# Kernel optimization log

Hardware: AMD Instinct MI355X
Metric: run time of the kernel (lower is better)

Reference implementation:

```python
import jax, jax.numpy as jnp
import numpy as np

V, H, B, S, T = 512, 1024, 128, 256, 128


def setup_inputs() -> dict:
    key = jax.random.key(0)
    ks = jax.random.split(key, 16)
    s = 1.0 / np.sqrt(H)
    f32 = jnp.float32
    return {
        "encoder_outputs": jax.random.normal(ks[0], (B, S, H), f32),
        "encoder_hidden": jax.random.normal(ks[1], (1, B, H), f32),
        "encoder_cell": jax.random.normal(ks[2], (1, B, H), f32),
        "target_tensor": jax.random.randint(ks[3], (B, T), 0, V),
        "max_length": T,
        "emb": (jax.random.normal(ks[4], (V, H), f32) * s),
        "Wa_w": jax.random.normal(ks[5], (H, H), f32) * s,
        "Wa_b": jnp.zeros((H,), f32),
        "Ua_w": jax.random.normal(ks[6], (H, H), f32) * s,
        "Ua_b": jnp.zeros((H,), f32),
        "Va_w": jax.random.normal(ks[7], (1, H), f32) * s,
        "Va_b": jnp.zeros((1,), f32),
        "W_ih": jax.random.normal(ks[8], (4 * H, 2 * H), f32) * s,
        "W_hh": jax.random.normal(ks[9], (4 * H, H), f32) * s,
        "b_ih": jnp.zeros((4 * H,), f32),
        "b_hh": jnp.zeros((4 * H,), f32),
        "out_w": jax.random.normal(ks[10], (V, H), f32) * s,
        "out_b": jnp.zeros((V,), f32),
    }


def reference(encoder_outputs, encoder_hidden, encoder_cell, target_tensor, max_length,
              emb, Wa_w, Wa_b, Ua_w, Ua_b, Va_w, Va_b,
              W_ih, W_hh, b_ih, b_hh, out_w, out_b):
    # Teacher forcing: decoder input at step i is SOS (=0) then target[:, i-1].
    bsz = encoder_outputs.shape[0]
    sos = jnp.zeros((bsz, 1), dtype=target_tensor.dtype)
    tokens = jnp.concatenate([sos, target_tensor[:, : max_length - 1]], axis=1)  # [B, T]
    xs = emb[tokens].transpose(1, 0, 2)  # [T, B, H] (dropout = identity, eval mode)

    # Ua(keys) is loop-invariant (original recomputes it each step; same math).
    keys_proj = jnp.einsum('bsh,kh->bsk', encoder_outputs, Ua_w) + Ua_b  # [B, S, H]

    def step(carry, emb_t):
        h, c = carry  # [B, H] each
        q = h @ Wa_w.T + Wa_b  # Bahdanau query projection [B, H]
        e = jnp.tanh(q[:, None, :] + keys_proj) @ Va_w[0] + Va_b[0]  # [B, S]
        w = jax.nn.softmax(e, axis=-1)
        ctx = jnp.einsum('bs,bsh->bh', w, encoder_outputs)
        x = jnp.concatenate([emb_t, ctx], axis=-1)  # [B, 2H]
        gates = x @ W_ih.T + b_ih + h @ W_hh.T + b_hh  # [B, 4H], torch order i,f,g,o
        i, f, g, o = jnp.split(gates, 4, axis=-1)
        c_new = jax.nn.sigmoid(f) * c + jax.nn.sigmoid(i) * jnp.tanh(g)
        h_new = jax.nn.sigmoid(o) * jnp.tanh(c_new)
        logits = h_new @ out_w.T + out_b  # [B, V]
        return (h_new, c_new), (logits, w)

    init = (encoder_hidden[0], encoder_cell[0])
    (h_fin, c_fin), (logits, attn) = jax.lax.scan(step, init, xs)
    log_probs = jax.nn.log_softmax(logits.transpose(1, 0, 2), axis=-1)  # [B, T, V]
    return log_probs, h_fin[None], attn.transpose(1, 0, 2)  # hidden [1,B,H], attn [B,T,S]
```

## Files before the change

kernel.cpp:

```cpp
#include <hip/hip_runtime.h>

#define B_ 128
#define S_ 256
#define H_ 1024
#define V_ 512
#define T_ 128
#define G4 4096

typedef __attribute__((ext_vector_type(8))) short bf16x8;
typedef __attribute__((ext_vector_type(4))) float f32x4;
typedef __attribute__((ext_vector_type(2))) float f32x2;

__device__ __forceinline__ float bf2f(unsigned short x) {
    unsigned int u = ((unsigned int)x) << 16;
    return __builtin_bit_cast(float, u);
}
__device__ __forceinline__ unsigned short f2b(float f) {
    unsigned int u = __builtin_bit_cast(unsigned int, f);
    u = u + 0x7fffu + ((u >> 16) & 1u);
    return (unsigned short)(u >> 16);
}
__device__ __forceinline__ float ftanh(float x) {
    float e = __expf(2.f * x);
    return 1.f - 2.f * __builtin_amdgcn_rcpf(e + 1.f);
}
__device__ __forceinline__ float fsigm(float x) {
    return __builtin_amdgcn_rcpf(1.f + __expf(-x));
}
__device__ __forceinline__ void gll16(const void* g, void* l) {
    __builtin_amdgcn_global_load_lds(
        (const __attribute__((address_space(1))) unsigned int*)g,
        (__attribute__((address_space(3))) unsigned int*)l, 16, 0, 0);
}

__device__ __forceinline__ unsigned char sw_e4m3(float f) {
    unsigned int ub = __builtin_bit_cast(unsigned int, f);
    unsigned char s = (unsigned char)((ub >> 24) & 0x80);
    float a = fabsf(f);
    if (!(a < 464.f)) return (unsigned char)(s | 0x7E);
    if (a < 0.0009765625f) return s;
    if (a < 0.015625f) {
        int m = (int)(a * 512.f + 0.5f);
        if (m >= 8) return (unsigned char)(s | 0x08);
        return (unsigned char)(s | m);
    }
    unsigned int u = __builtin_bit_cast(unsigned int, a);
    u += 0x7FFFF + ((u >> 20) & 1);
    int e = (int)(u >> 23) - 127;
    if (e > 8) return (unsigned char)(s | 0x7E);
    unsigned int man = (u >> 20) & 7;
    return (unsigned char)(s | ((unsigned int)(e + 7) << 3) | man);
}
__device__ __forceinline__ float sw_f_e4m3(unsigned int byte) {
    unsigned int s = (byte & 0x80u) << 24;
    unsigned int em = byte & 0x7Fu;
    float v;
    if (em >= 8u) v = __builtin_bit_cast(float, (em + 960u) << 20);
    else v = (float)em * 0.001953125f;
    return __builtin_bit_cast(float, __builtin_bit_cast(unsigned int, v) | s);
}
__device__ __forceinline__ unsigned char enc1(float a) {
#if __has_builtin(__builtin_amdgcn_cvt_pk_fp8_f32)
    unsigned int w = __builtin_amdgcn_cvt_pk_fp8_f32(a, a, 0u, false);
    return (unsigned char)(w & 0xff);
#else
    return sw_e4m3(a);
#endif
}
__device__ __forceinline__ unsigned int enc4(float a, float b, float c, float d) {
#if __has_builtin(__builtin_amdgcn_cvt_pk_fp8_f32)
    unsigned int w = 0;
    w = __builtin_amdgcn_cvt_pk_fp8_f32(a, b, w, false);
    w = __builtin_amdgcn_cvt_pk_fp8_f32(c, d, w, true);
    return w;
#else
    return (unsigned int)sw_e4m3(a) | ((unsigned int)sw_e4m3(b) << 8) |
           ((unsigned int)sw_e4m3(c) << 16) | ((unsigned int)sw_e4m3(d) << 24);
#endif
}
__device__ __forceinline__ void dec4(unsigned int w, float* o) {
#if __has_builtin(__builtin_amdgcn_cvt_pk_f32_fp8)
    f32x2 lo = __builtin_amdgcn_cvt_pk_f32_fp8(w, false);
    f32x2 hi = __builtin_amdgcn_cvt_pk_f32_fp8(w, true);
    o[0] = lo.x; o[1] = lo.y; o[2] = hi.x; o[3] = hi.y;
#else
    o[0] = sw_f_e4m3(w & 0xff); o[1] = sw_f_e4m3((w >> 8) & 0xff);
    o[2] = sw_f_e4m3((w >> 16) & 0xff); o[3] = sw_f_e4m3(w >> 24);
#endif
}

__global__ void f32_to_bf16_x4(const float4* __restrict__ in, ushort4* __restrict__ out, int n4) {
    int i = blockIdx.x * 256 + threadIdx.x;
    if (i < n4) {
        float4 v = in[i];
        ushort4 o;
        o.x = f2b(v.x); o.y = f2b(v.y); o.z = f2b(v.z); o.w = f2b(v.w);
        out[i] = o;
    }
}

__global__ void f32_to_fp8_x4(const float4* __restrict__ in, unsigned int* __restrict__ out, int n4) {
    int i = blockIdx.x * 256 + threadIdx.x;
    if (i < n4) {
        float4 v = in[i];
        out[i] = enc4(v.x, v.y, v.z, v.w);
    }
}

__global__ void cvt_gather(const float* __restrict__ src, int src_ld, int coff,
                           unsigned short* __restrict__ dst, int perm) {
    int i = blockIdx.x * 256 + threadIdx.x;
    int r = i >> 8;
    int c = (i & 255) * 4;
    int sr = perm ? (((r & 3) << 10) + (r >> 2)) : r;
    float4 v = *reinterpret_cast<const float4*>(src + (size_t)sr * src_ld + coff + c);
    ushort4 o;
    o.x = f2b(v.x); o.y = f2b(v.y); o.z = f2b(v.z); o.w = f2b(v.w);
    *reinterpret_cast<ushort4*>(dst + (size_t)r * 1024 + c) = o;
}

__global__ void build_toks(const int* __restrict__ target, int* __restrict__ toks) {
    int idx = blockIdx.x * 256 + threadIdx.x;
    if (idx < T_ * B_) {
        int t = idx / B_, b = idx % B_;
        toks[idx] = (t == 0) ? 0 : target[b * T_ + t - 1];
    }
}

__global__ void build_bsum(const float* __restrict__ b_ih, const float* __restrict__ b_hh,
                           float* __restrict__ bsum) {
    int j = blockIdx.x * 256 + threadIdx.x;
    if (j < G4) {
        int pj = ((j & 3) << 10) + (j >> 2);
        bsum[j] = b_ih[pj] + b_hh[pj];
    }
}

template<int MODE>
__global__ __launch_bounds__(256) void gemm_mf(
    const unsigned short* __restrict__ A,
    const unsigned short* __restrict__ Bw,
    int K, int ldb, int ldc,
    float* __restrict__ C, unsigned char* __restrict__ C8,
    const float* __restrict__ bias)
{
    __shared__ unsigned short As[2 * 8192];
    __shared__ unsigned short Bs[2 * 8192];
    const int tid = threadIdx.x;
    const int lane = tid & 63;
    const int wv = tid >> 6;
    const int m0 = blockIdx.x * 64;
    const int n0 = blockIdx.y * 64;

    const unsigned short* ga[4];
    const unsigned short* gb[4];
    #pragma unroll
    for (int j = 0; j < 4; ++j) {
        int ci = tid + 256 * j;
        int row = ci >> 4;
        int src = (ci & 15) ^ (row & 7);
        ga[j] = A + (size_t)(m0 + row) * K + src * 8;
        gb[j] = Bw + (size_t)(n0 + row) * ldb + src * 8;
    }

    f32x4 acc[2][2] = {};
    const int r0 = (wv >> 1) * 32;
    const int cq0 = (wv & 1) * 32;
    const int fr = lane & 15;
    const int kg = lane >> 4;

    auto stage = [&](int k0, int p) {
        #pragma unroll
        for (int j = 0; j < 4; ++j) {
            gll16(ga[j] + k0, As + p * 8192 + j * 2048 + wv * 512);
            gll16(gb[j] + k0, Bs + p * 8192 + j * 2048 + wv * 512);
        }
    };

    stage(0, 0);
    stage(128, 1);
    int p = 0;
    for (int k0 = 0; k0 < K; k0 += 128) {
        if (k0 + 128 < K) {
            asm volatile("s_waitcnt vmcnt(8)" ::: "memory");
        } else {
            asm volatile("s_waitcnt vmcnt(0)" ::: "memory");
        }
        __builtin_amdgcn_sched_barrier(0);
        __builtin_amdgcn_s_barrier();
        __builtin_amdgcn_sched_barrier(0);
        const unsigned short* Ab = As + p * 8192;
        const unsigned short* Bb = Bs + p * 8192;
        bf16x8 af[2][4], bfr[2][4];
        #pragma unroll
        for (int f = 0; f < 2; ++f)
            #pragma unroll
            for (int kh = 0; kh < 4; ++kh) {
                int ra = r0 + f * 16 + fr;
                af[f][kh] = *(const bf16x8*)&Ab[ra * 128 + (((kh * 4 + kg) ^ (ra & 7)) << 3)];
                int rb = cq0 + f * 16 + fr;
                bfr[f][kh] = *(const bf16x8*)&Bb[rb * 128 + (((kh * 4 + kg) ^ (rb & 7)) << 3)];
            }
        asm volatile("s_waitcnt lgkmcnt(0)" ::: "memory");
        __builtin_amdgcn_sched_barrier(0);
        __builtin_amdgcn_s_barrier();
        __builtin_amdgcn_sched_barrier(0);
        if (k0 + 256 < K) stage(k0 + 256, p);
        __builtin_amdgcn_s_setprio(1);
        #pragma unroll
        for (int f = 0; f < 2; ++f)
            #pragma unroll
            for (int g = 0; g < 2; ++g)
                #pragma unroll
                for (int kh = 0; kh < 4; ++kh)
                    acc[f][g] = __builtin_amdgcn_mfma_f32_16x16x32_bf16(
                        af[f][kh], bfr[g][kh], acc[f][g], 0, 0, 0);
        __builtin_amdgcn_s_setprio(0);
        p ^= 1;
    }

    const int erow = (lane >> 4) * 4;
    const int ecol = lane & 15;
    #pragma unroll
    for (int f = 0; f < 2; ++f) {
        #pragma unroll
        for (int g = 0; g < 2; ++g) {
            #pragma unroll
            for (int r = 0; r < 4; ++r) {
                int row = m0 + r0 + f * 16 + erow + r;
                int col = n0 + cq0 + g * 16 + ecol;
                float v = acc[f][g][r] + bias[col];
                if (MODE == 0) C[(size_t)row * ldc + col] = v;
                else C8[(size_t)row * ldc + col] = enc1(v);
            }
        }
    }
}

template<int MODE>
__global__ __launch_bounds__(256) void gemm_n32(
    const unsigned short* __restrict__ A,
    const unsigned short* __restrict__ Bw,
    int K, int ldb, int ldc,
    float* __restrict__ C, unsigned short* __restrict__ Cb,
    const float* __restrict__ bias,
    const float* __restrict__ Pemb,
    const int* __restrict__ toks,
    float* __restrict__ Cq,
    float* __restrict__ Lg,
    int flag)
{
    __shared__ unsigned short As[3 * 8192];
    __shared__ unsigned short Bs[3 * 4096];
    const int tid = threadIdx.x;
    const int lane = tid & 63;
    const int wv = tid >> 6;
    const int m0 = blockIdx.x * 64;
    const int n0 = blockIdx.y * 32;

    const unsigned short* ga[4];
    const unsigned short* gb[2];
    #pragma unroll
    for (int j = 0; j < 4; ++j) {
        int ci = tid + 256 * j;
        int row = ci >> 4;
        int src = (ci & 15) ^ (row & 7);
        ga[j] = A + (size_t)(m0 + row) * K + src * 8;
    }
    #pragma unroll
    for (int j = 0; j < 2; ++j) {
        int ci = tid + 256 * j;
        int row = ci >> 4;
        int src = (ci & 15) ^ (row & 7);
        gb[j] = Bw + (size_t)(n0 + row) * ldb + src * 8;
    }

    f32x4 acc[2] = {};
    const int r0 = (wv >> 1) * 32;
    const int c0 = (wv & 1) * 16;
    const int fr = lane & 15;
    const int kg = lane >> 4;

    auto stage = [&](int k0, int p) {
        #pragma unroll
        for (int j = 0; j < 4; ++j)
            gll16(ga[j] + k0, As + p * 8192 + j * 2048 + wv * 512);
        #pragma unroll
        for (int j = 0; j < 2; ++j)
            gll16(gb[j] + k0, Bs + p * 4096 + j * 2048 + wv * 512);
    };

    stage(0, 0);
    stage(128, 1);
    stage(256, 2);
    int p = 0;
    for (int k0 = 0; k0 < K; k0 += 128) {
        if (k0 + 256 < K) {
            asm volatile("s_waitcnt vmcnt(12)" ::: "memory");
        } else if (k0 + 128 < K) {
            asm volatile("s_waitcnt vmcnt(6)" ::: "memory");
        } else {
            asm volatile("s_waitcnt vmcnt(0)" ::: "memory");
        }
        __builtin_amdgcn_sched_barrier(0);
        __builtin_amdgcn_s_barrier();
        __builtin_amdgcn_sched_barrier(0);
        const unsigned short* Ab = As + p * 8192;
        const unsigned short* Bb = Bs + p * 4096;
        bf16x8 af[2][4], bfr[4];
        #pragma unroll
        for (int kh = 0; kh < 4; ++kh) {
            #pragma unroll
            for (int f = 0; f < 2; ++f) {
                int ra = r0 + f * 16 + fr;
                af[f][kh] = *(const bf16x8*)&Ab[ra * 128 + (((kh * 4 + kg) ^ (ra & 7)) << 3)];
            }
            int rb = c0 + fr;
            bfr[kh] = *(const bf16x8*)&Bb[rb * 128 + (((kh * 4 + kg) ^ (rb & 7)) << 3)];
        }
        asm volatile("s_waitcnt lgkmcnt(0)" ::: "memory");
        __builtin_amdgcn_sched_barrier(0);
        __builtin_amdgcn_s_barrier();
        __builtin_amdgcn_sched_barrier(0);
        if (k0 + 384 < K) stage(k0 + 384, p);
        __builtin_amdgcn_s_setprio(1);
        #pragma unroll
        for (int f = 0; f < 2; ++f)
            #pragma unroll
            for (int kh = 0; kh < 4; ++kh)
                acc[f] = __builtin_amdgcn_mfma_f32_16x16x32_bf16(
                    af[f][kh], bfr[kh], acc[f], 0, 0, 0);
        __builtin_amdgcn_s_setprio(0);
        p = (p == 2) ? 0 : p + 1;
    }

    const int erow = (lane >> 4) * 4;
    const int ecol = lane & 15;

    if constexpr (MODE == 4) {
        __shared__ float Lt[64 * 32];
        __syncthreads();
        #pragma unroll
        for (int f = 0; f < 2; ++f)
            #pragma unroll
            for (int r = 0; r < 4; ++r)
                Lt[(r0 + f * 16 + erow + r) * 32 + c0 + ecol] = acc[f][r];
        __syncthreads();
        #pragma unroll
        for (int i = 0; i < 2; ++i) {
            int pi = tid + 256 * i;
            int r = pi >> 3, u = pi & 7;
            int b = m0 + r;
            int hh = (n0 >> 2) + u;
            f32x4 gv = *reinterpret_cast<const f32x4*>(&Lt[r * 32 + u * 4]);
            const float* gp = C + (size_t)b * G4 + n0 + u * 4;
            float iv = gv[0] + gp[0];
            float fv = gv[1] + gp[1];
            float gg = gv[2] + gp[2];
            float ov = gv[3] + gp[3];
            int ci = b * H_ + hh;
            float cn = fsigm(fv) * Cq[ci] + fsigm(iv) * ftanh(gg);
            float hn = fsigm(ov) * ftanh(cn);
            Cq[ci] = cn;
            Cb[ci] = f2b(hn);
            if (flag) Lg[ci] = hn;
        }
    } else {
        #pragma unroll
        for (int f = 0; f < 2; ++f) {
            #pragma unroll
            for (int r = 0; r < 4; ++r) {
                int row = m0 + r0 + f * 16 + erow + r;
                int col = n0 + c0 + ecol;
                float v = acc[f][r];
                if (MODE == 0) {
                    C[(size_t)row * ldc + col] = v + bias[col];
                } else {
                    if (col < H_) {
                        Cq[(size_t)row * H_ + col] = v + bias[col];
                    } else {
                        int cg = col - H_;
                        C[(size_t)row * G4 + cg] = v + Pemb[(size_t)toks[row] * G4 + cg];
                    }
                }
            }
        }
    }
}

__global__ __launch_bounds__(256) void attn_e(
    const unsigned int* __restrict__ kp8,
    const float* __restrict__ q,
    const float* __restrict__ Va,
    const unsigned int* __restrict__ encb8,
    float* __restrict__ es_g,
    unsigned short* __restrict__ pctx)
{
    const int b = blockIdx.x;
    const int sh = blockIdx.y;
    const int tid = threadIdx.x;
    const int lane = tid & 63;
    const int wv = tid >> 6;
    __shared__ float qs[H_];
    __shared__ float vas[H_];
    __shared__ float pe[16];

    *reinterpret_cast<float4*>(&qs[tid * 4]) =
        *reinterpret_cast<const float4*>(&q[(size_t)b * H_ + tid * 4]);
    *reinterpret_cast<float4*>(&vas[tid * 4]) =
        *reinterpret_cast<const float4*>(&Va[tid * 4]);
    __syncthreads();

    #pragma unroll
    for (int si = 0; si < 4; ++si) {
        int s_loc = wv * 4 + si;
        const uint4* kr = reinterpret_cast<const uint4*>(
            kp8 + (size_t)(b * S_ + sh * 16 + s_loc) * 256);
        uint4 u = kr[lane];
        const int h0 = lane * 16;
        float d[4];
        float acc = 0.f;
        dec4(u.x, d);
        acc += vas[h0 + 0] * ftanh(qs[h0 + 0] + d[0]);
        acc += vas[h0 + 1] * ftanh(qs[h0 + 1] + d[1]);
        acc += vas[h0 + 2] * ftanh(qs[h0 + 2] + d[2]);
        acc += vas[h0 + 3] * ftanh(qs[h0 + 3] + d[3]);
        dec4(u.y, d);
        acc += vas[h0 + 4] * ftanh(qs[h0 + 4] + d[0]);
        acc += vas[h0 + 5] * ftanh(qs[h0 + 5] + d[1]);
        acc += vas[h0 + 6] * ftanh(qs[h0 + 6] + d[2]);
        acc += vas[h0 + 7] * ftanh(qs[h0 + 7] + d[3]);
        dec4(u.z, d);
        acc += vas[h0 + 8] * ftanh(qs[h0 + 8] + d[0]);
        acc += vas[h0 + 9] * ftanh(qs[h0 + 9] + d[1]);
        acc += vas[h0 + 10] * ftanh(qs[h0 + 10] + d[2]);
        acc += vas[h0 + 11] * ftanh(qs[h0 + 11] + d[3]);
        dec4(u.w, d);
        acc += vas[h0 + 12] * ftanh(qs[h0 + 12] + d[0]);
        acc += vas[h0 + 13] * ftanh(qs[h0 + 13] + d[1]);
        acc += vas[h0 + 14] * ftanh(qs[h0 + 14] + d[2]);
        acc += vas[h0 + 15] * ftanh(qs[h0 + 15] + d[3]);
        #pragma unroll
        for (int off = 32; off; off >>= 1) acc += __shfl_down(acc, off);
        if (lane == 0) {
            pe[s_loc] = __expf(acc);
            es_g[(size_t)b * S_ + sh * 16 + s_loc] = acc;
        }
    }
    __syncthreads();

    const int c0 = tid * 4;
    float ax = 0.f, ay = 0.f, az = 0.f, aw = 0.f;
    #pragma unroll
    for (int sl = 0; sl < 16; ++sl) {
        unsigned int u = encb8[(size_t)(b * S_ + sh * 16 + sl) * 256 + tid];
        float d[4];
        dec4(u, d);
        float w = pe[sl];
        ax += w * d[0];
        ay += w * d[1];
        az += w * d[2];
        aw += w * d[3];
    }
    ushort4 o4;
    o4.x = f2b(ax); o4.y = f2b(ay); o4.z = f2b(az); o4.w = f2b(aw);
    *reinterpret_cast<ushort4*>(&pctx[((size_t)b * 16 + sh) * H_ + c0]) = o4;
}

__global__ __launch_bounds__(256) void attn_comb(
    const float* __restrict__ es_g,
    const unsigned short* __restrict__ pctx,
    unsigned short* __restrict__ ctxb,
    float* __restrict__ attnOut,
    int t)
{
    const int b = blockIdx.x;
    const int hh = blockIdx.y;
    const int tid = threadIdx.x;
    const int lane = tid & 63;
    const int wv = tid >> 6;
    __shared__ float reds[4];

    float ex = __expf(es_g[(size_t)b * S_ + tid]);
    float sm = ex;
    #pragma unroll
    for (int off = 32; off; off >>= 1) sm += __shfl_xor(sm, off);
    if (lane == 0) reds[wv] = sm;
    __syncthreads();
    sm = reds[0] + reds[1] + reds[2] + reds[3];
    float rZ = __builtin_amdgcn_rcpf(sm);
    if (hh == 0) attnOut[((size_t)(b * T_ + t)) * S_ + tid] = ex * rZ;

    const int c0 = hh * 512 + tid * 2;
    float a0 = 0.f, a1 = 0.f;
    #pragma unroll
    for (int blk = 0; blk < 16; ++blk) {
        ushort2 pv = *reinterpret_cast<const ushort2*>(
            &pctx[((size_t)b * 16 + blk) * H_ + c0]);
        a0 += bf2f(pv.x); a1 += bf2f(pv.y);
    }
    ushort2 o; o.x = f2b(a0 * rZ); o.y = f2b(a1 * rZ);
    *reinterpret_cast<ushort2*>(&ctxb[(size_t)b * H_ + c0]) = o;
}

__global__ __launch_bounds__(256) void lsm_all(
    const float* __restrict__ lgall,
    float* __restrict__ lp)
{
    int r = blockIdx.x;
    int t = r >> 7, b = r & (B_ - 1);
    int tid = threadIdx.x;
    int lane = tid & 63, wv = tid >> 6;
    __shared__ float red[4];
    float a0 = lgall[(size_t)r * V_ + tid];
    float a1 = lgall[(size_t)r * V_ + 256 + tid];
    float mx = fmaxf(a0, a1);
    #pragma unroll
    for (int off = 32; off; off >>= 1) mx = fmaxf(mx, __shfl_xor(mx, off));
    if (lane == 0) red[wv] = mx;
    __syncthreads();
    mx = fmaxf(fmaxf(red[0], red[1]), fmaxf(red[2], red[3]));
    float sm = __expf(a0 - mx) + __expf(a1 - mx);
    #pragma unroll
    for (int off = 32; off; off >>= 1) sm += __shfl_xor(sm, off);
    __syncthreads();
    if (lane == 0) red[wv] = sm;
    __syncthreads();
    sm = red[0] + red[1] + red[2] + red[3];
    float lse = mx + __logf(sm);
    size_t off = ((size_t)b * T_ + t) * V_;
    lp[off + tid] = a0 - lse;
    lp[off + tid + 256] = a1 - lse;
}

extern "C" void kernel_launch(void* const* d_in, const int* in_sizes, int n_in,
                              void* d_out, int out_size, void* d_ws, size_t ws_size,
                              hipStream_t stream) {
    const float* enc   = (const float*)d_in[0];
    const float* h0    = (const float*)d_in[1];
    const float* c0    = (const float*)d_in[2];
    const int*   targ  = (const int*)d_in[3];
    const float* emb   = (const float*)d_in[5];
    const float* Wa_w  = (const float*)d_in[6];
    const float* Wa_b  = (const float*)d_in[7];
    const float* Ua_w  = (const float*)d_in[8];
    const float* Ua_b  = (const float*)d_in[9];
    const float* Va_w  = (const float*)d_in[10];
    const float* W_ih  = (const float*)d_in[12];
    const float* W_hh  = (const float*)d_in[13];
    const float* b_ih  = (const float*)d_in[14];
    const float* b_hh  = (const float*)d_in[15];
    const float* out_w = (const float*)d_in[16];
    const float* out_b = (const float*)d_in[17];

    float* out  = (float*)d_out;
    float* lp   = out;
    float* hid  = out + (size_t)B_ * T_ * V_;
    float* attn = hid + (size_t)B_ * H_;

    char* w = (char*)d_ws;
    auto alloc = [&](size_t bytes) {
        char* p = w;
        w += (bytes + 255) & ~(size_t)255;
        return p;
    };
    const size_t NKP = (size_t)B_ * S_ * H_;
    unsigned int* kp8      = (unsigned int*)alloc(NKP);
    unsigned int* encb8    = (unsigned int*)alloc(NKP);
    char* uni = alloc(NKP * 2);
    unsigned short* encb = (unsigned short*)uni;
    unsigned short* hall = (unsigned short*)uni;
    float* lgall = (float*)(uni + (size_t)T_ * B_ * H_ * 2);
    unsigned short* Wcat_b = (unsigned short*)alloc((size_t)5120 * H_ * 2);
    unsigned short* Wih1_b = (unsigned short*)alloc((size_t)G4 * H_ * 2);
    unsigned short* Wih2_b = (unsigned short*)alloc((size_t)G4 * H_ * 2);
    unsigned short* Uaw_b  = (unsigned short*)alloc((size_t)H_ * H_ * 2);
    unsigned short* emb_b  = (unsigned short*)alloc((size_t)V_ * H_ * 2);
    unsigned short* owb_b  = (unsigned short*)alloc((size_t)V_ * H_ * 2);
    unsigned short* hb0    = (unsigned short*)alloc((size_t)B_ * H_ * 2);
    unsigned short* ctxb   = (unsigned short*)alloc((size_t)B_ * H_ * 2);
    float* Pemb  = (float*)alloc((size_t)V_ * G4 * 4);
    float* bsumP = (float*)alloc((size_t)G4 * 4);
    int*   toks  = (int*)alloc((size_t)T_ * B_ * 4);
    float* cbuf  = (float*)alloc((size_t)B_ * H_ * 4);
    float* qbuf  = (float*)alloc((size_t)B_ * H_ * 4);
    float* gates = (float*)alloc((size_t)B_ * G4 * 4);
    float* es_g  = (float*)alloc((size_t)B_ * S_ * 4);
    unsigned short* pctx = (unsigned short*)alloc((size_t)B_ * 16 * H_ * 2);
    if ((size_t)(w - (char*)d_ws) > ws_size) return;

    auto cvt = [&](const float* src, unsigned short* dst, size_t n) {
        int n4 = (int)(n / 4);
        f32_to_bf16_x4<<<(n4 + 255) / 256, 256, 0, stream>>>((const float4*)src, (ushort4*)dst, n4);
    };

    cvt(enc, encb, NKP);
    f32_to_fp8_x4<<<(int)(NKP / 4 + 255) / 256, 256, 0, stream>>>(
        (const float4*)enc, encb8, (int)(NKP / 4));
    cvt(Ua_w, Uaw_b, (size_t)H_ * H_);
    cvt(emb, emb_b, (size_t)V_ * H_);
    cvt(h0, hb0, (size_t)B_ * H_);
    cvt_gather<<<1024, 256, 0, stream>>>(Wa_w, H_, 0, Wcat_b, 0);
    cvt_gather<<<4096, 256, 0, stream>>>(W_hh, H_, 0, Wcat_b + (size_t)1024 * H_, 1);
    cvt_gather<<<512, 256, 0, stream>>>(out_w, H_, 0, owb_b, 0);
    cvt_gather<<<4096, 256, 0, stream>>>(W_ih, 2 * H_, 0, Wih1_b, 1);
    cvt_gather<<<4096, 256, 0, stream>>>(W_ih, 2 * H_, H_, Wih2_b, 1);
    build_toks<<<(T_ * B_ + 255) / 256, 256, 0, stream>>>(targ, toks);
    build_bsum<<<(G4 + 255) / 256, 256, 0, stream>>>(b_ih, b_hh, bsumP);
    hipMemcpyAsync(cbuf, c0, (size_t)B_ * H_ * 4, hipMemcpyDeviceToDevice, stream);

    gemm_mf<1><<<dim3((B_ * S_) / 64, H_ / 64), 256, 0, stream>>>(
        encb, Uaw_b, H_, H_, H_, nullptr, (unsigned char*)kp8, Ua_b);
    gemm_mf<0><<<dim3(V_ / 64, G4 / 64), 256, 0, stream>>>(
        emb_b, Wih1_b, H_, H_, G4, Pemb, nullptr, bsumP);

    for (int t = 0; t < T_; ++t) {
        const unsigned short* hprev = (t == 0) ? hb0 : hall + (size_t)(t - 1) * B_ * H_;
        gemm_n32<2><<<dim3(2, 160), 256, 0, stream>>>(
            hprev, Wcat_b, H_, H_, 0, gates, nullptr, Wa_b,
            Pemb, toks + t * B_, qbuf, nullptr, 0);
        attn_e<<<dim3(B_, 16), 256, 0, stream>>>(kp8, qbuf, Va_w, encb8, es_g, pctx);
        attn_comb<<<dim3(B_, 2), 256, 0, stream>>>(es_g, pctx, ctxb, attn, t);
        gemm_n32<4><<<dim3(2, 128), 256, 0, stream>>>(
            ctxb, Wih2_b, H_, H_, 0, gates, hall + (size_t)t * B_ * H_, nullptr,
            nullptr, nullptr, cbuf, hid, t == T_ - 1);
    }

    gemm_n32<0><<<dim3((T_ * B_) / 64, V_ / 32), 256, 0, stream>>>(
        hall, owb_b, H_, H_, V_, lgall, nullptr, out_b,
        nullptr, nullptr, nullptr, nullptr, 0);
    lsm_all<<<T_ * B_, 256, 0, stream>>>(lgall, lp);
}
```

Before: 5.612 ms.

## Fuse attention score, softmax and context into one kernel per batch half

Replaces the two-kernel attention (partial scores/context per 16-position slice, then a combine kernel) with a single kernel where each block handles one batch row and half of the hidden dimension, computing all 256 scores, the softmax and the context in place. This removes one launch per decoder step and the global round trip through partial-context and score buffers. The score/tanh work is now duplicated across the two half-blocks per batch row, and the grid shrinks from 2048 to 256 blocks, reducing parallelism.

```diff
diff --git a/kernel.cpp b/kernel.cpp
--- a/kernel.cpp
+++ b/kernel.cpp
@@ -388,35 +388,36 @@
     }
 }
 
-__global__ __launch_bounds__(256) void attn_e(
+__global__ __launch_bounds__(512) void attn_fused(
     const unsigned int* __restrict__ kp8,
     const float* __restrict__ q,
     const float* __restrict__ Va,
     const unsigned int* __restrict__ encb8,
-    float* __restrict__ es_g,
-    unsigned short* __restrict__ pctx)
+    unsigned short* __restrict__ ctxb,
+    float* __restrict__ attnOut,
+    int t)
 {
-    const int b = blockIdx.x;
-    const int sh = blockIdx.y;
+    const int b = blockIdx.x >> 1;
+    const int hh = blockIdx.x & 1;
     const int tid = threadIdx.x;
     const int lane = tid & 63;
     const int wv = tid >> 6;
     __shared__ float qs[H_];
     __shared__ float vas[H_];
-    __shared__ float pe[16];
-
-    *reinterpret_cast<float4*>(&qs[tid * 4]) =
-        *reinterpret_cast<const float4*>(&q[(size_t)b * H_ + tid * 4]);
-    *reinterpret_cast<float4*>(&vas[tid * 4]) =
-        *reinterpret_cast<const float4*>(&Va[tid * 4]);
-    __syncthreads();
-
-    #pragma unroll
-    for (int si = 0; si < 4; ++si) {
-        int s_loc = wv * 4 + si;
-        const uint4* kr = reinterpret_cast<const uint4*>(
-            kp8 + (size_t)(b * S_ + sh * 16 + s_loc) * 256);
-        uint4 u = kr[lane];
+    __shared__ float es[S_];
+    __shared__ float red[8];
+    __shared__ float part[4][128][4];
+
+    *reinterpret_cast<float2*>(&qs[tid * 2]) =
+        *reinterpret_cast<const float2*>(&q[(size_t)b * H_ + tid * 2]);
+    *reinterpret_cast<float2*>(&vas[tid * 2]) =
+        *reinterpret_cast<const float2*>(&Va[tid * 2]);
+    __syncthreads();
+
+    for (int si = 0; si < 32; ++si) {
+        int s = wv * 32 + si;
+        uint4 u = reinterpret_cast<const uint4*>(
+            kp8 + (size_t)(b * S_ + s) * 256)[lane];
         const int h0 = lane * 16;
         float d[4];
         float acc = 0.f;
@@ -442,65 +443,56 @@
         acc += vas[h0 + 15] * ftanh(qs[h0 + 15] + d[3]);
         #pragma unroll
         for (int off = 32; off; off >>= 1) acc += __shfl_down(acc, off);
-        if (lane == 0) {
-            pe[s_loc] = __expf(acc);
-            es_g[(size_t)b * S_ + sh * 16 + s_loc] = acc;
-        }
-    }
-    __syncthreads();
-
-    const int c0 = tid * 4;
-    float ax = 0.f, ay = 0.f, az = 0.f, aw = 0.f;
-    #pragma unroll
-    for (int sl = 0; sl < 16; ++sl) {
-        unsigned int u = encb8[(size_t)(b * S_ + sh * 16 + sl) * 256 + tid];
+        if (lane == 0) es[s] = acc;
+    }
+    __syncthreads();
+
+    float ex = (tid < S_) ? __expf(es[tid]) : 0.f;
+    float sm = ex;
+    #pragma unroll
+    for (int off = 32; off; off >>= 1) sm += __shfl_xor(sm, off);
+    if (lane == 0) red[wv] = sm;
+    __syncthreads();
+    sm = 0.f;
+    #pragma unroll
+    for (int i = 0; i < 8; ++i) sm += red[i];
+    float rZ = __builtin_amdgcn_rcpf(sm);
+    if (tid < S_) {
+        es[tid] = ex;
+        if (hh == 0) attnOut[((size_t)(b * T_ + t)) * S_ + tid] = ex * rZ;
+    }
+    __syncthreads();
+
+    const int w = tid & 127;
+    const int sq = tid >> 7;
+    const int gw = hh * 128 + w;
+    float a0 = 0.f, a1 = 0.f, a2 = 0.f, a3 = 0.f;
+    const unsigned int* ep = encb8 + (size_t)(b * S_ + sq * 64) * 256 + gw;
+    #pragma unroll 4
+    for (int s = 0; s < 64; ++s) {
+        unsigned int u = ep[(size_t)s * 256];
         float d[4];
         dec4(u, d);
-        float w = pe[sl];
-        ax += w * d[0];
-        ay += w * d[1];
-        az += w * d[2];
-        aw += w * d[3];
-    }
-    ushort4 o4;
-    o4.x = f2b(ax); o4.y = f2b(ay); o4.z = f2b(az); o4.w = f2b(aw);
-    *reinterpret_cast<ushort4*>(&pctx[((size_t)b * 16 + sh) * H_ + c0]) = o4;
-}
-
-__global__ __launch_bounds__(256) void attn_comb(
-    const float* __restrict__ es_g,
-    const unsigned short* __restrict__ pctx,
-    unsigned short* __restrict__ ctxb,
-    float* __restrict__ attnOut,
-    int t)
-{
-    const int b = blockIdx.x;
-    const int hh = blockIdx.y;
-    const int tid = threadIdx.x;
-    const int lane = tid & 63;
-    const int wv = tid >> 6;
-    __shared__ float reds[4];
-
-    float ex = __expf(es_g[(size_t)b * S_ + tid]);
-    float sm = ex;
-    #pragma unroll
-    for (int off = 32; off; off >>= 1) sm += __shfl_xor(sm, off);
-    if (lane == 0) reds[wv] = sm;
-    __syncthreads();
-    sm = reds[0] + reds[1] + reds[2] + reds[3];
-    float rZ = __builtin_amdgcn_rcpf(sm);
-    if (hh == 0) attnOut[((size_t)(b * T_ + t)) * S_ + tid] = ex * rZ;
-
-    const int c0 = hh * 512 + tid * 2;
-    float a0 = 0.f, a1 = 0.f;
-    #pragma unroll
-    for (int blk = 0; blk < 16; ++blk) {
-        ushort2 pv = *reinterpret_cast<const ushort2*>(
-            &pctx[((size_t)b * 16 + blk) * H_ + c0]);
-        a0 += bf2f(pv.x); a1 += bf2f(pv.y);
-    }
-    ushort2 o; o.x = f2b(a0 * rZ); o.y = f2b(a1 * rZ);
-    *reinterpret_cast<ushort2*>(&ctxb[(size_t)b * H_ + c0]) = o;
+        float wt = es[sq * 64 + s];
+        a0 += wt * d[0];
+        a1 += wt * d[1];
+        a2 += wt * d[2];
+        a3 += wt * d[3];
+    }
+    part[sq][w][0] = a0; part[sq][w][1] = a1; part[sq][w][2] = a2; part[sq][w][3] = a3;
+    __syncthreads();
+    if (tid < 128) {
+        f32x4 c4 = *reinterpret_cast<const f32x4*>(part[0][tid]);
+        #pragma unroll
+        for (int qd = 1; qd < 4; ++qd) {
+            f32x4 pv = *reinterpret_cast<const f32x4*>(part[qd][tid]);
+            c4[0] += pv[0]; c4[1] += pv[1]; c4[2] += pv[2]; c4[3] += pv[3];
+        }
+        ushort4 o;
+        o.x = f2b(c4[0] * rZ); o.y = f2b(c4[1] * rZ);
+        o.z = f2b(c4[2] * rZ); o.w = f2b(c4[3] * rZ);
+        *reinterpret_cast<ushort4*>(&ctxb[(size_t)b * H_ + hh * 512 + tid * 4]) = o;
+    }
 }
 
 __global__ __launch_bounds__(256) void lsm_all(
@@ -585,8 +577,6 @@
     float* cbuf  = (float*)alloc((size_t)B_ * H_ * 4);
     float* qbuf  = (float*)alloc((size_t)B_ * H_ * 4);
     float* gates = (float*)alloc((size_t)B_ * G4 * 4);
-    float* es_g  = (float*)alloc((size_t)B_ * S_ * 4);
-    unsigned short* pctx = (unsigned short*)alloc((size_t)B_ * 16 * H_ * 2);
     if ((size_t)(w - (char*)d_ws) > ws_size) return;
 
     auto cvt = [&](const float* src, unsigned short* dst, size_t n) {
@@ -619,8 +609,7 @@
         gemm_n32<2><<<dim3(2, 160), 256, 0, stream>>>(
             hprev, Wcat_b, H_, H_, 0, gates, nullptr, Wa_b,
             Pemb, toks + t * B_, qbuf, nullptr, 0);
-        attn_e<<<dim3(B_, 16), 256, 0, stream>>>(kp8, qbuf, Va_w, encb8, es_g, pctx);
-        attn_comb<<<dim3(B_, 2), 256, 0, stream>>>(es_g, pctx, ctxb, attn, t);
+        attn_fused<<<256, 512, 0, stream>>>(kp8, qbuf, Va_w, encb8, ctxb, attn, t);
         gemm_n32<4><<<dim3(2, 128), 256, 0, stream>>>(
             ctxb, Wih2_b, H_, H_, 0, gates, hall + (size_t)t * B_ * H_, nullptr,
             nullptr, nullptr, cbuf, hid, t == T_ - 1);
```

New measurement: 7.582 ms. 35.1% more time.
